# Kernel optimization log

Measured on AMD Instinct MI355X. Metric: run time of the kernel, lower is better.

Reference implementation:

```python
import jax, jax.numpy as jnp
import numpy as np

C = 512          # channels
NH = 8           # num_heads
ENC = 512        # encoder_channels
SCALE_P = 1.0    # channels_scale_for_positional_embedding
CP = int(C * SCALE_P)
GROUPS = 32


def group_norm(x, g, b, eps=1e-5):
    # x: (N, C, L); GroupNorm32 computes stats in fp32
    N, Ch, L = x.shape
    xg = x.reshape(N, GROUPS, Ch // GROUPS, L).astype(jnp.float32)
    mu = xg.mean(axis=(2, 3), keepdims=True)
    var = xg.var(axis=(2, 3), keepdims=True)
    xn = ((xg - mu) * jax.lax.rsqrt(var + eps)).reshape(N, Ch, L).astype(x.dtype)
    return xn * g[None, :, None] + b[None, :, None]


def conv1(x, W, b):
    # 1x1 conv1d: x (N, Cin, L), W (Cout, Cin), b (Cout)
    return jnp.einsum('oc,ncl->nol', W, x) + b[None, :, None]


def setup_inputs() -> dict:
    key = jax.random.key(0)
    ks = iter(jax.random.split(key, 40))
    rn = lambda *s: jax.random.normal(next(ks), s, dtype=jnp.float32)
    inp = {
        'x': rn(8, C, 32, 32),
        'xf_out': rn(8, ENC, 64),
        'obj_contour_embedding': rn(8, ENC, 64),
        'obj_description_embedding': rn(8, ENC, 64),
        'image_patch_contour_embedding': rn(8, ENC, 1024),
        # norm_for_qkv
        'gn_qkv_g': jnp.ones(C), 'gn_qkv_b': jnp.zeros(C),
        # projectors (1x1 conv weights); zero_module proj_out given random weights for a meaningful baseline
        'W_self_qkv': rn(3 * C, C) * 0.02, 'b_self_qkv': jnp.zeros(3 * C),
        'W_cross_q': rn(C, C) * 0.02, 'b_cross_q': jnp.zeros(C),
        'W_content': rn(2 * C, ENC) * 0.02, 'b_content': jnp.zeros(2 * C),
        'W_pos': rn(CP, ENC) * 0.02, 'b_pos': jnp.zeros(CP),
        'gn_desc_g': jnp.ones(ENC), 'gn_desc_b': jnp.zeros(ENC),
        'gn_cpos_g': jnp.ones(CP), 'gn_cpos_b': jnp.zeros(CP),
        'gn_ipos_g': jnp.ones(CP), 'gn_ipos_b': jnp.zeros(CP),
        'W_self_out': rn(C, C) * 0.02, 'b_self_out': jnp.zeros(C),
        'W_cross_out': rn(C, C) * 0.02, 'b_cross_out': jnp.zeros(C),
    }
    return inp


def _attn(q, k, v, scale):
    # q,k: (B, Cq, T/S), v: (B, Cv, S)
    w = jnp.einsum('bct,bcs->bts', q * scale, k * scale)
    w = jax.nn.softmax(w.astype(jnp.float32), axis=-1).astype(q.dtype)
    return jnp.einsum('bts,bcs->bct', w, v)


def reference(x, xf_out, obj_contour_embedding, obj_description_embedding,
              image_patch_contour_embedding,
              gn_qkv_g, gn_qkv_b, W_self_qkv, b_self_qkv, W_cross_q, b_cross_q,
              W_content, b_content, W_pos, b_pos,
              gn_desc_g, gn_desc_b, gn_cpos_g, gn_cpos_b, gn_ipos_g, gn_ipos_b,
              W_self_out, b_self_out, W_cross_out, b_cross_out):
    b_, c_, h_, w_ = x.shape
    xf = x.reshape(b_, c_, -1)                      # (N, C, L1)
    L1 = xf.shape[-1]
    L2 = obj_contour_embedding.shape[-1]
    dc = C // NH
    dp = CP // NH
    scale = float(int((1 + SCALE_P) * C) // NH) ** -0.25

    # ---- self-attention over image patches ----
    qkv = conv1(group_norm(xf, gn_qkv_g, gn_qkv_b), W_self_qkv, b_self_qkv)
    sq, sk, sv = jnp.split(qkv, 3, axis=1)
    sq = sq.reshape(b_ * NH, dc, L1)
    sk = sk.reshape(b_ * NH, dc, L1)
    sv = sv.reshape(b_ * NH, dc, L1)

    ipos = conv1(image_patch_contour_embedding, W_pos, b_pos)
    ipos = group_norm(ipos, gn_ipos_g, gn_ipos_b)
    ipos = ipos.reshape(b_ * NH, dp, L1)

    sq = jnp.concatenate([sq, ipos], axis=1)
    sk = jnp.concatenate([sk, ipos], axis=1)
    self_out = _attn(sq, sk, sv, scale).reshape(b_, C, L1)
    self_out = conv1(self_out, W_self_out, b_self_out)
    xf = xf + self_out

    # ---- cross-attention to object tokens ----
    cq = conv1(group_norm(xf, gn_qkv_g, gn_qkv_b), W_cross_q, b_cross_q)
    cq = cq.reshape(b_ * NH, dc, L1)
    cq = jnp.concatenate([cq, ipos], axis=1)

    cpos = conv1(obj_contour_embedding, W_pos, b_pos)
    cpos = group_norm(cpos, gn_cpos_g, gn_cpos_b)
    cpos = cpos.reshape(b_ * NH, dp, L2)

    content = (xf_out + group_norm(obj_description_embedding, gn_desc_g, gn_desc_b)) / 2
    kv = conv1(content, W_content, b_content)
    ck, cv = jnp.split(kv, 2, axis=1)
    ck = ck.reshape(b_ * NH, dc, L2)
    cv = cv.reshape(b_ * NH, dc, L2)
    ck = jnp.concatenate([ck, cpos], axis=1)

    cross_out = _attn(cq, ck, cv, scale).reshape(b_, C, L1)
    cross_out = conv1(cross_out, W_cross_out, b_cross_out)

    return (xf + cross_out).reshape(b_, c_, h_, w_)
```

## Files before the change

### kernel.cpp

```cpp
#include <hip/hip_runtime.h>

typedef unsigned short u16;
typedef __attribute__((ext_vector_type(8))) short bf16x8;
typedef __attribute__((ext_vector_type(4))) float f32x4;

__device__ __forceinline__ float bf2f(u16 u) {
  union { unsigned int i; float f; } v;
  v.i = ((unsigned int)u) << 16;
  return v.f;
}
__device__ __forceinline__ u16 f2bf(float f) {
  union { float f; unsigned int i; } v;
  v.f = f;
  unsigned int r = v.i + 0x7FFFu + ((v.i >> 16) & 1u);
  return (u16)(r >> 16);
}

__device__ __forceinline__ float4 ld4f(const float* p) {
  return *reinterpret_cast<const float4*>(p);
}
__device__ __forceinline__ float4 ld4f(const u16* p) {
  uint2 v = *reinterpret_cast<const uint2*>(p);
  float4 r;
  r.x = bf2f((u16)(v.x & 0xffff)); r.y = bf2f((u16)(v.x >> 16));
  r.z = bf2f((u16)(v.y & 0xffff)); r.w = bf2f((u16)(v.y >> 16));
  return r;
}

template <typename TIN>
__global__ __launch_bounds__(1024) void gn_kernel(
    const TIN* __restrict__ In, u16* __restrict__ OutBuf,
    const float* __restrict__ G, const float* __restrict__ Bt,
    const float* __restrict__ Add, float post_scale,
    int C, int L, int cpg)
{
  const int blk = blockIdx.x;
  const int n = blk >> 5, grp = blk & 31;
  const size_t base = ((size_t)n * C + (size_t)grp * cpg) * L;
  const int cnt = cpg * L;
  const int cnt4 = cnt >> 2;
  const int tid = threadIdx.x;

  float s = 0.f, s2 = 0.f;
  for (int i = tid; i < cnt4; i += 1024) {
    float4 v = ld4f(In + base + (size_t)i * 4);
    s += v.x + v.y + v.z + v.w;
    s2 += v.x * v.x + v.y * v.y + v.z * v.z + v.w * v.w;
  }
#pragma unroll
  for (int d = 1; d < 64; d <<= 1) {
    s += __shfl_xor(s, d);
    s2 += __shfl_xor(s2, d);
  }
  __shared__ float ps[16], ps2[16], stat[2];
  const int wid = tid >> 6;
  if ((tid & 63) == 0) { ps[wid] = s; ps2[wid] = s2; }
  __syncthreads();
  if (tid == 0) {
    float a = 0.f, b2 = 0.f;
#pragma unroll
    for (int w = 0; w < 16; ++w) { a += ps[w]; b2 += ps2[w]; }
    const float mean = a / cnt;
    const float var = b2 / cnt - mean * mean;
    stat[0] = mean;
    stat[1] = rsqrtf(var + 1e-5f);
  }
  __syncthreads();
  const float mean = stat[0], rstd = stat[1];

  for (int i = tid; i < cnt4; i += 1024) {
    const int i4 = i * 4;
    const int ch = grp * cpg + i4 / L;
    float4 v = ld4f(In + base + i4);
    const float g = G[ch] * rstd, bt = Bt[ch] - mean * rstd * G[ch];
    float4 r;
    r.x = v.x * g + bt; r.y = v.y * g + bt;
    r.z = v.z * g + bt; r.w = v.w * g + bt;
    if (Add) {
      float4 a = *reinterpret_cast<const float4*>(Add + base + i4);
      r.x = (r.x + a.x) * post_scale; r.y = (r.y + a.y) * post_scale;
      r.z = (r.z + a.z) * post_scale; r.w = (r.w + a.w) * post_scale;
    }
    uint2 o;
    o.x = (unsigned int)f2bf(r.x) | ((unsigned int)f2bf(r.y) << 16);
    o.y = (unsigned int)f2bf(r.z) | ((unsigned int)f2bf(r.w) << 16);
    *reinterpret_cast<uint2*>(OutBuf + base + i4) = o;
  }
}

__device__ __forceinline__ void load4(const u16* p, u16* d) {
  uint2 v = *reinterpret_cast<const uint2*>(p);
  d[0] = (u16)(v.x & 0xffff); d[1] = (u16)(v.x >> 16);
  d[2] = (u16)(v.y & 0xffff); d[3] = (u16)(v.y >> 16);
}
__device__ __forceinline__ void load4(const float* p, u16* d) {
  float4 v = *reinterpret_cast<const float4*>(p);
  d[0] = f2bf(v.x); d[1] = f2bf(v.y); d[2] = f2bf(v.z); d[3] = f2bf(v.w);
}

template <typename TX, int LT>
__global__ __launch_bounds__(256) void gemm_conv(
    const TX* __restrict__ X, const float* __restrict__ W,
    const float* __restrict__ Bias,
    u16* __restrict__ OutBf, float* __restrict__ Out32,
    const float* __restrict__ Res,
    int Cin, int L, int O, int mode)
{
  constexpr int NL = LT / 16;
  __shared__ __align__(16) u16 As[64][40];
  __shared__ __align__(16) u16 Bs[LT][40];
  const int tid = threadIdx.x;
  const int wave = tid >> 6;
  const int lane = tid & 63;
  const int n = blockIdx.z;
  const int o0 = blockIdx.x * 64;
  const int l0 = blockIdx.y * LT;
  const TX* Xn = X + (size_t)n * Cin * L;

  const int ao = tid >> 2, akc = (tid & 3) * 8;
  const int c2 = (tid & 15) * 2, lt0 = (tid >> 4) * NL;
  const float* wp = W + (size_t)(o0 + ao) * Cin + akc;
  const TX* xp0 = Xn + (size_t)c2 * L + l0 + lt0;
  const TX* xp1 = xp0 + L;

  f32x4 acc[NL];
#pragma unroll
  for (int i = 0; i < NL; ++i) acc[i] = (f32x4){0.f, 0.f, 0.f, 0.f};

  const int row = lane & 15;
  const int kh = (lane >> 4) * 8;

  float4 wa = *reinterpret_cast<const float4*>(wp);
  float4 wb = *reinterpret_cast<const float4*>(wp + 4);
  u16 blo[NL], bhi[NL];
#pragma unroll
  for (int ch = 0; ch < NL; ch += 4) {
    load4(xp0 + ch, blo + ch);
    load4(xp1 + ch, bhi + ch);
  }

  const int nK = Cin >> 5;
  for (int kt = 0; kt < nK; ++kt) {
    {
      union { uint4 q; u16 u[8]; } ap;
      ap.u[0] = f2bf(wa.x); ap.u[1] = f2bf(wa.y);
      ap.u[2] = f2bf(wa.z); ap.u[3] = f2bf(wa.w);
      ap.u[4] = f2bf(wb.x); ap.u[5] = f2bf(wb.y);
      ap.u[6] = f2bf(wb.z); ap.u[7] = f2bf(wb.w);
      *reinterpret_cast<uint4*>(&As[ao][akc]) = ap.q;
    }
#pragma unroll
    for (int j = 0; j < NL; ++j)
      *reinterpret_cast<unsigned int*>(&Bs[lt0 + j][c2]) =
          (unsigned int)blo[j] | ((unsigned int)bhi[j] << 16);
    __syncthreads();

    if (kt + 1 < nK) {
      const int k0 = (kt + 1) * 32;
      wa = *reinterpret_cast<const float4*>(wp + k0);
      wb = *reinterpret_cast<const float4*>(wp + k0 + 4);
#pragma unroll
      for (int ch = 0; ch < NL; ch += 4) {
        load4(xp0 + (size_t)k0 * L + ch, blo + ch);
        load4(xp1 + (size_t)k0 * L + ch, bhi + ch);
      }
    }

    bf16x8 a = *reinterpret_cast<const bf16x8*>(&As[wave * 16 + row][kh]);
#pragma unroll
    for (int lt = 0; lt < NL; ++lt) {
      bf16x8 b = *reinterpret_cast<const bf16x8*>(&Bs[lt * 16 + row][kh]);
      acc[lt] = __builtin_amdgcn_mfma_f32_16x16x32_bf16(a, b, acc[lt], 0, 0, 0);
    }
    __syncthreads();
  }

  const int col = lane & 15;
  const int r0 = (lane >> 4) * 4;
#pragma unroll
  for (int lt = 0; lt < NL; ++lt) {
    const int ll = l0 + lt * 16 + col;
#pragma unroll
    for (int j = 0; j < 4; ++j) {
      const int oo = o0 + wave * 16 + r0 + j;
      float v = acc[lt][j] + Bias[oo];
      const size_t idx = ((size_t)n * O + oo) * L + ll;
      if (mode == 1) {
        Out32[idx] = v + Res[idx];
      } else {
        OutBf[idx] = f2bf(v);
      }
    }
  }
}

__global__ __launch_bounds__(256, 2) void flash_attn(
    const u16* __restrict__ qA, int qA_C, int qA_off,
    const u16* __restrict__ qB,
    const u16* __restrict__ kA, int kA_C, int kA_off,
    const u16* __restrict__ kB,
    const u16* __restrict__ V, int v_C, int v_off,
    u16* __restrict__ Out, int S_len, float qscale)
{
  __shared__ __align__(16) u16 Qs[128 * 128];
  __shared__ __align__(16) u16 Ks[64 * 128];
  __shared__ __align__(16) u16 Ps[128 * 64];
  __shared__ __align__(16) u16 Vt[64 * 64];

  const int tid = threadIdx.x;
  const int wave = tid >> 6, lane = tid & 63;
  const int b = blockIdx.y >> 3, h = blockIdx.y & 7;
  const int t0 = blockIdx.x * 128;
  const int l16 = lane & 15, q4 = lane >> 4;
  const int swz = (l16 & 7) << 3;

  const int c2 = (tid & 63) * 2;
  const u16* q0 = (c2 < 64)
      ? qA + ((size_t)b * qA_C + qA_off + h * 64 + c2) * 1024 + t0
      : qB + ((size_t)b * 512 + h * 64 + (c2 - 64)) * 1024 + t0;
  const u16* q1 = q0 + 1024;
  const u16* k0 = (c2 < 64)
      ? kA + ((size_t)b * kA_C + kA_off + h * 64 + c2) * (size_t)S_len
      : kB + ((size_t)b * 512 + h * 64 + (c2 - 64)) * (size_t)S_len;
  const u16* k1 = k0 + S_len;
  const u16* vb = V + ((size_t)b * v_C + v_off + h * 64) * (size_t)S_len;

  const int s8 = (tid >> 6) * 8;
  const int cv0 = tid >> 3, sb0 = (tid & 7) * 8;
  const int cv1 = (tid + 256) >> 3, sb1 = sb0;

  uint4 kr0a = *reinterpret_cast<const uint4*>(k0 + s8);
  uint4 kr0c = *reinterpret_cast<const uint4*>(k1 + s8);
  uint4 kr1a = *reinterpret_cast<const uint4*>(k0 + s8 + 32);
  uint4 kr1c = *reinterpret_cast<const uint4*>(k1 + s8 + 32);
  uint4 vr0 = *reinterpret_cast<const uint4*>(vb + (size_t)cv0 * S_len + sb0);
  uint4 vr1 = *reinterpret_cast<const uint4*>(vb + (size_t)cv1 * S_len + sb1);

#pragma unroll
  for (int it = 0; it < 4; ++it) {
    const int t8 = (tid >> 6) * 8 + it * 32;
    union { uint4 q; u16 u[8]; } a, c;
    a.q = *reinterpret_cast<const uint4*>(q0 + t8);
    c.q = *reinterpret_cast<const uint4*>(q1 + t8);
#pragma unroll
    for (int j = 0; j < 8; ++j) {
      const unsigned int lo = f2bf(bf2f(a.u[j]) * qscale);
      const unsigned int hi = f2bf(bf2f(c.u[j]) * qscale);
      *reinterpret_cast<unsigned int*>(&Qs[(t8 + j) * 128 + (c2 ^ (j << 3))]) =
          lo | (hi << 16);
    }
  }
  __syncthreads();

  bf16x8 qf[2][4];
#pragma unroll
  for (int g = 0; g < 2; ++g)
#pragma unroll
    for (int kk = 0; kk < 4; ++kk)
      qf[g][kk] = *reinterpret_cast<const bf16x8*>(
          &Qs[(wave * 32 + g * 16 + l16) * 128 + ((kk * 32 + q4 * 8) ^ swz)]);

  float m_run[2][4], l_run[2][4];
  f32x4 o_acc[2][4];
#pragma unroll
  for (int g = 0; g < 2; ++g)
#pragma unroll
    for (int j = 0; j < 4; ++j) {
      m_run[g][j] = -1e30f; l_run[g][j] = 0.f;
      o_acc[g][j] = (f32x4){0.f, 0.f, 0.f, 0.f};
    }

  const int NT = S_len >> 6;
  for (int t = 0; t < NT; ++t) {
    {
      union { uint4 q; u16 u[8]; } a, c;
      a.q = kr0a; c.q = kr0c;
#pragma unroll
      for (int j = 0; j < 8; ++j)
        *reinterpret_cast<unsigned int*>(&Ks[(s8 + j) * 128 + (c2 ^ (j << 3))]) =
            (unsigned int)a.u[j] | ((unsigned int)c.u[j] << 16);
      a.q = kr1a; c.q = kr1c;
#pragma unroll
      for (int j = 0; j < 8; ++j)
        *reinterpret_cast<unsigned int*>(&Ks[(s8 + 32 + j) * 128 + (c2 ^ (j << 3))]) =
            (unsigned int)a.u[j] | ((unsigned int)c.u[j] << 16);
    }
    *reinterpret_cast<uint4*>(&Vt[cv0 * 64 + (sb0 ^ ((cv0 & 7) << 3))]) = vr0;
    *reinterpret_cast<uint4*>(&Vt[cv1 * 64 + (sb1 ^ ((cv1 & 7) << 3))]) = vr1;
    __syncthreads();

    if (t + 1 < NT) {
      const int sc = (t + 1) * 64;
      kr0a = *reinterpret_cast<const uint4*>(k0 + sc + s8);
      kr0c = *reinterpret_cast<const uint4*>(k1 + sc + s8);
      kr1a = *reinterpret_cast<const uint4*>(k0 + sc + s8 + 32);
      kr1c = *reinterpret_cast<const uint4*>(k1 + sc + s8 + 32);
      vr0 = *reinterpret_cast<const uint4*>(vb + (size_t)cv0 * S_len + sc + sb0);
      vr1 = *reinterpret_cast<const uint4*>(vb + (size_t)cv1 * S_len + sc + sb1);
    }

    f32x4 sacc[2][4];
#pragma unroll
    for (int g = 0; g < 2; ++g)
#pragma unroll
      for (int st = 0; st < 4; ++st) sacc[g][st] = (f32x4){0.f, 0.f, 0.f, 0.f};
#pragma unroll
    for (int st = 0; st < 4; ++st) {
#pragma unroll
      for (int kk = 0; kk < 4; ++kk) {
        bf16x8 kf = *reinterpret_cast<const bf16x8*>(
            &Ks[(st * 16 + l16) * 128 + ((kk * 32 + q4 * 8) ^ swz)]);
        sacc[0][st] = __builtin_amdgcn_mfma_f32_16x16x32_bf16(qf[0][kk], kf, sacc[0][st], 0, 0, 0);
        sacc[1][st] = __builtin_amdgcn_mfma_f32_16x16x32_bf16(qf[1][kk], kf, sacc[1][st], 0, 0, 0);
      }
    }

    float corr[2][4];
#pragma unroll
    for (int g = 0; g < 2; ++g) {
      float mt[4];
#pragma unroll
      for (int j = 0; j < 4; ++j)
        mt[j] = fmaxf(fmaxf(sacc[g][0][j], sacc[g][1][j]),
                      fmaxf(sacc[g][2][j], sacc[g][3][j]));
#pragma unroll
      for (int d = 1; d < 16; d <<= 1)
#pragma unroll
        for (int j = 0; j < 4; ++j) mt[j] = fmaxf(mt[j], __shfl_xor(mt[j], d));

      float ls[4];
#pragma unroll
      for (int j = 0; j < 4; ++j) {
        const float mn = fmaxf(m_run[g][j], mt[j]);
        corr[g][j] = exp2f(m_run[g][j] - mn);
        m_run[g][j] = mn;
        ls[j] = 0.f;
      }
      float pv[4][4];
#pragma unroll
      for (int st = 0; st < 4; ++st)
#pragma unroll
        for (int j = 0; j < 4; ++j) {
          pv[st][j] = exp2f(sacc[g][st][j] - m_run[g][j]);
          ls[j] += pv[st][j];
        }
#pragma unroll
      for (int d = 1; d < 16; d <<= 1)
#pragma unroll
        for (int j = 0; j < 4; ++j) ls[j] += __shfl_xor(ls[j], d);
#pragma unroll
      for (int j = 0; j < 4; ++j) l_run[g][j] = l_run[g][j] * corr[g][j] + ls[j];

#pragma unroll
      for (int st = 0; st < 4; ++st)
#pragma unroll
        for (int j = 0; j < 4; ++j)
          Ps[(wave * 32 + g * 16 + q4 * 4 + j) * 64 +
             ((st * 16 + l16) ^ (((q4 * 4 + j) & 7) << 3))] = f2bf(pv[st][j]);

#pragma unroll
      for (int ct = 0; ct < 4; ++ct)
#pragma unroll
        for (int j = 0; j < 4; ++j) o_acc[g][ct][j] *= corr[g][j];
    }

    bf16x8 pa[2][2];
#pragma unroll
    for (int g = 0; g < 2; ++g)
#pragma unroll
      for (int ks = 0; ks < 2; ++ks)
        pa[g][ks] = *reinterpret_cast<const bf16x8*>(
            &Ps[(wave * 32 + g * 16 + l16) * 64 + ((ks * 32 + q4 * 8) ^ swz)]);
#pragma unroll
    for (int ct = 0; ct < 4; ++ct) {
#pragma unroll
      for (int ks = 0; ks < 2; ++ks) {
        bf16x8 vf = *reinterpret_cast<const bf16x8*>(
            &Vt[(ct * 16 + l16) * 64 + ((ks * 32 + q4 * 8) ^ swz)]);
        o_acc[0][ct] = __builtin_amdgcn_mfma_f32_16x16x32_bf16(pa[0][ks], vf, o_acc[0][ct], 0, 0, 0);
        o_acc[1][ct] = __builtin_amdgcn_mfma_f32_16x16x32_bf16(pa[1][ks], vf, o_acc[1][ct], 0, 0, 0);
      }
    }
    __syncthreads();
  }

#pragma unroll
  for (int g = 0; g < 2; ++g) {
    float inv[4];
#pragma unroll
    for (int j = 0; j < 4; ++j) inv[j] = 1.f / l_run[g][j];
    const size_t obase =
        ((size_t)b * 512 + h * 64) * 1024 + t0 + wave * 32 + g * 16 + q4 * 4;
#pragma unroll
    for (int ct = 0; ct < 4; ++ct) {
      union { unsigned long long d; u16 u[4]; } pk;
#pragma unroll
      for (int j = 0; j < 4; ++j) pk.u[j] = f2bf(o_acc[g][ct][j] * inv[j]);
      *reinterpret_cast<unsigned long long*>(
          Out + obase + (size_t)(ct * 16 + l16) * 1024) = pk.d;
    }
  }
}

extern "C" void kernel_launch(void* const* d_in, const int* in_sizes, int n_in,
                              void* d_out, int out_size, void* d_ws, size_t ws_size,
                              hipStream_t stream) {
  const float* X_in        = (const float*)d_in[0];
  const float* xf_out      = (const float*)d_in[1];
  const float* obj_cont    = (const float*)d_in[2];
  const float* obj_desc    = (const float*)d_in[3];
  const float* ipce        = (const float*)d_in[4];
  const float* gn_qkv_g    = (const float*)d_in[5];
  const float* gn_qkv_b    = (const float*)d_in[6];
  const float* W_self_qkv  = (const float*)d_in[7];
  const float* b_self_qkv  = (const float*)d_in[8];
  const float* W_cross_q   = (const float*)d_in[9];
  const float* b_cross_q   = (const float*)d_in[10];
  const float* W_content   = (const float*)d_in[11];
  const float* b_content   = (const float*)d_in[12];
  const float* W_pos       = (const float*)d_in[13];
  const float* b_pos       = (const float*)d_in[14];
  const float* gn_desc_g   = (const float*)d_in[15];
  const float* gn_desc_b   = (const float*)d_in[16];
  const float* gn_cpos_g   = (const float*)d_in[17];
  const float* gn_cpos_b   = (const float*)d_in[18];
  const float* gn_ipos_g   = (const float*)d_in[19];
  const float* gn_ipos_b   = (const float*)d_in[20];
  const float* W_self_out  = (const float*)d_in[21];
  const float* b_self_out  = (const float*)d_in[22];
  const float* W_cross_out = (const float*)d_in[23];
  const float* b_cross_out = (const float*)d_in[24];

  char* base = (char*)d_ws;
  u16* A = (u16*)base;
  u16* B = (u16*)(base + 8 * 1024 * 1024);
  u16* C = (u16*)(base + 32 * 1024 * 1024);
  u16* D = (u16*)(base + 40 * 1024 * 1024);

  u16* norm1 = A;
  u16* norm2 = A;
  u16* cposr   = A;
  u16* cpos    = A + 262144;
  u16* content = A + 2 * 262144;
  u16* kvbuf   = A + 3 * 262144;
  u16* qkv  = B;
  u16* cq   = B;
  u16* ipos = C;
  u16* iposr = D;
  u16* attn1 = D;
  u16* cattn = D;
  float* xf32 = (float*)d_out;
  float* outp = (float*)d_out;

  const float qscale = 0.08838834764831845f * 1.4426950408889634f;
  dim3 blk(256);
  dim3 blkgn(1024);

  gn_kernel<float><<<dim3(256), blkgn, 0, stream>>>(X_in, norm1, gn_qkv_g, gn_qkv_b,
                                                    nullptr, 1.f, 512, 1024, 16);
  gemm_conv<u16, 128><<<dim3(24, 8, 8), blk, 0, stream>>>(norm1, W_self_qkv, b_self_qkv,
                                                          qkv, nullptr, nullptr,
                                                          512, 1024, 1536, 0);
  gemm_conv<float, 128><<<dim3(8, 8, 8), blk, 0, stream>>>(ipce, W_pos, b_pos, iposr,
                                                           nullptr, nullptr,
                                                           512, 1024, 512, 0);
  gn_kernel<u16><<<dim3(256), blkgn, 0, stream>>>(iposr, ipos, gn_ipos_g, gn_ipos_b,
                                                  nullptr, 1.f, 512, 1024, 16);
  flash_attn<<<dim3(8, 64), blk, 0, stream>>>(qkv, 1536, 0, ipos,
                                              qkv, 1536, 512, ipos,
                                              qkv, 1536, 1024,
                                              attn1, 1024, qscale);
  gemm_conv<u16, 128><<<dim3(8, 8, 8), blk, 0, stream>>>(attn1, W_self_out, b_self_out,
                                                         nullptr, xf32, X_in,
                                                         512, 1024, 512, 1);
  gn_kernel<float><<<dim3(256), blkgn, 0, stream>>>(xf32, norm2, gn_qkv_g, gn_qkv_b,
                                                    nullptr, 1.f, 512, 1024, 16);
  gemm_conv<u16, 128><<<dim3(8, 8, 8), blk, 0, stream>>>(norm2, W_cross_q, b_cross_q, cq,
                                                         nullptr, nullptr,
                                                         512, 1024, 512, 0);
  gemm_conv<float, 64><<<dim3(8, 1, 8), blk, 0, stream>>>(obj_cont, W_pos, b_pos, cposr,
                                                          nullptr, nullptr,
                                                          512, 64, 512, 0);
  gn_kernel<u16><<<dim3(256), blkgn, 0, stream>>>(cposr, cpos, gn_cpos_g, gn_cpos_b,
                                                  nullptr, 1.f, 512, 64, 16);
  gn_kernel<float><<<dim3(256), blkgn, 0, stream>>>(obj_desc, content, gn_desc_g,
                                                    gn_desc_b, xf_out, 0.5f, 512, 64, 16);
  gemm_conv<u16, 64><<<dim3(16, 1, 8), blk, 0, stream>>>(content, W_content, b_content,
                                                         kvbuf, nullptr, nullptr,
                                                         512, 64, 1024, 0);
  flash_attn<<<dim3(8, 64), blk, 0, stream>>>(cq, 512, 0, ipos,
                                              kvbuf, 1024, 0, cpos,
                                              kvbuf, 1024, 512,
                                              cattn, 64, qscale);
  gemm_conv<u16, 128><<<dim3(8, 8, 8), blk, 0, stream>>>(cattn, W_cross_out, b_cross_out,
                                                         nullptr, outp, xf32,
                                                         512, 1024, 512, 1);
}
```

Measured before the change: 275.6 us.

## Load Q fragments directly from global, drop Qs LDS, raise occupancy

Removes the 32KB Q shared-memory staging buffer and its barrier by having each lane gather its Q MFMA fragment straight from global memory with scalar bf16 loads, scaling on the fly. With LDS use cut, launch bounds are raised from 2 to 4 blocks per CU to increase occupancy. MFMA sections are also wrapped in s_setprio to favour the matrix-issuing waves. The cost is strided, uncoalesced 2-byte global loads for Q (one per element across channels), and a tighter register budget under the higher launch bound that may cause spills.

```diff
diff --git a/kernel.cpp b/kernel.cpp
--- a/kernel.cpp
+++ b/kernel.cpp
@@ -194,7 +194,7 @@
   }
 }
 
-__global__ __launch_bounds__(256, 2) void flash_attn(
+__global__ __launch_bounds__(256, 4) void flash_attn(
     const u16* __restrict__ qA, int qA_C, int qA_off,
     const u16* __restrict__ qB,
     const u16* __restrict__ kA, int kA_C, int kA_off,
@@ -202,7 +202,6 @@
     const u16* __restrict__ V, int v_C, int v_off,
     u16* __restrict__ Out, int S_len, float qscale)
 {
-  __shared__ __align__(16) u16 Qs[128 * 128];
   __shared__ __align__(16) u16 Ks[64 * 128];
   __shared__ __align__(16) u16 Ps[128 * 64];
   __shared__ __align__(16) u16 Vt[64 * 64];
@@ -215,10 +214,6 @@
   const int swz = (l16 & 7) << 3;
 
   const int c2 = (tid & 63) * 2;
-  const u16* q0 = (c2 < 64)
-      ? qA + ((size_t)b * qA_C + qA_off + h * 64 + c2) * 1024 + t0
-      : qB + ((size_t)b * 512 + h * 64 + (c2 - 64)) * 1024 + t0;
-  const u16* q1 = q0 + 1024;
   const u16* k0 = (c2 < 64)
       ? kA + ((size_t)b * kA_C + kA_off + h * 64 + c2) * (size_t)S_len
       : kB + ((size_t)b * 512 + h * 64 + (c2 - 64)) * (size_t)S_len;
@@ -236,29 +231,24 @@
   uint4 vr0 = *reinterpret_cast<const uint4*>(vb + (size_t)cv0 * S_len + sb0);
   uint4 vr1 = *reinterpret_cast<const uint4*>(vb + (size_t)cv1 * S_len + sb1);
 
-#pragma unroll
-  for (int it = 0; it < 4; ++it) {
-    const int t8 = (tid >> 6) * 8 + it * 32;
-    union { uint4 q; u16 u[8]; } a, c;
-    a.q = *reinterpret_cast<const uint4*>(q0 + t8);
-    c.q = *reinterpret_cast<const uint4*>(q1 + t8);
-#pragma unroll
-    for (int j = 0; j < 8; ++j) {
-      const unsigned int lo = f2bf(bf2f(a.u[j]) * qscale);
-      const unsigned int hi = f2bf(bf2f(c.u[j]) * qscale);
-      *reinterpret_cast<unsigned int*>(&Qs[(t8 + j) * 128 + (c2 ^ (j << 3))]) =
-          lo | (hi << 16);
-    }
-  }
-  __syncthreads();
-
   bf16x8 qf[2][4];
 #pragma unroll
-  for (int g = 0; g < 2; ++g)
-#pragma unroll
-    for (int kk = 0; kk < 4; ++kk)
-      qf[g][kk] = *reinterpret_cast<const bf16x8*>(
-          &Qs[(wave * 32 + g * 16 + l16) * 128 + ((kk * 32 + q4 * 8) ^ swz)]);
+  for (int g = 0; g < 2; ++g) {
+    const int t = t0 + wave * 32 + g * 16 + l16;
+#pragma unroll
+    for (int kk = 0; kk < 4; ++kk) {
+      union { bf16x8 v; u16 u[8]; } pk;
+#pragma unroll
+      for (int j = 0; j < 8; ++j) {
+        const int c = kk * 32 + q4 * 8 + j;
+        const u16* src = (c < 64)
+            ? qA + ((size_t)b * qA_C + qA_off + h * 64 + c) * 1024
+            : qB + ((size_t)b * 512 + h * 64 + (c - 64)) * 1024;
+        pk.u[j] = f2bf(bf2f(src[t]) * qscale);
+      }
+      qf[g][kk] = pk.v;
+    }
+  }
 
   float m_run[2][4], l_run[2][4];
   f32x4 o_acc[2][4];
@@ -304,6 +294,7 @@
     for (int g = 0; g < 2; ++g)
 #pragma unroll
       for (int st = 0; st < 4; ++st) sacc[g][st] = (f32x4){0.f, 0.f, 0.f, 0.f};
+    __builtin_amdgcn_s_setprio(1);
 #pragma unroll
     for (int st = 0; st < 4; ++st) {
 #pragma unroll
@@ -314,6 +305,7 @@
         sacc[1][st] = __builtin_amdgcn_mfma_f32_16x16x32_bf16(qf[1][kk], kf, sacc[1][st], 0, 0, 0);
       }
     }
+    __builtin_amdgcn_s_setprio(0);
 
     float corr[2][4];
 #pragma unroll
@@ -371,6 +363,7 @@
       for (int ks = 0; ks < 2; ++ks)
         pa[g][ks] = *reinterpret_cast<const bf16x8*>(
             &Ps[(wave * 32 + g * 16 + l16) * 64 + ((ks * 32 + q4 * 8) ^ swz)]);
+    __builtin_amdgcn_s_setprio(1);
 #pragma unroll
     for (int ct = 0; ct < 4; ++ct) {
 #pragma unroll
@@ -381,6 +374,7 @@
         o_acc[1][ct] = __builtin_amdgcn_mfma_f32_16x16x32_bf16(pa[1][ks], vf, o_acc[1][ct], 0, 0, 0);
       }
     }
+    __builtin_amdgcn_s_setprio(0);
     __syncthreads();
   }
 
```

Result: slower. 430.2 us (+56.1%).
